# Optimization experiments

Measured on AMD Instinct MI355X. Metric: run time of the kernel, lower is better.

## Reference

```python
import jax, jax.numpy as jnp
import numpy as np

HEADS, DIM_HEAD, DIM = 12, 64, 768
H = W = 32
N = H * W
B = 4


def _ln(x, g, b, eps=1e-5):
    mu = x.mean(-1, keepdims=True)
    var = ((x - mu) ** 2).mean(-1, keepdims=True)
    return (x - mu) / jnp.sqrt(var + eps) * g + b


def _get_epipolar(k, src_c2w, target_c2w, h=H, w=W):
    # Faithful port of Epipolar_Attention.get_epipolar, without the (hw*hw,3) repeat
    # materialization (uses broadcasting for the pairwise cross product instead).
    b = k.shape[0]
    Wf = h * 16.0 / 9.0
    k = k.astype(jnp.float32)
    k = k.at[:, 0, :].multiply(Wf).at[:, 1, :].multiply(float(h))
    k = k.at[:, 0, 2].set(h / 2.0).at[:, 1, 2].set(h / 2.0)
    ii, jj = jnp.meshgrid(jnp.arange(h), jnp.arange(w), indexing='ij')
    # after the torch column swap: (col, row, 1)
    coords = jnp.stack([jj.ravel(), ii.ravel(), jnp.ones(h * w, jnp.int32)], axis=1).astype(jnp.float32)  # [hw,3]
    k3 = k[:, :3, :3]
    src_r, src_t = src_c2w[:, :3, :3].astype(jnp.float32), src_c2w[:, :3, 3].astype(jnp.float32)
    tgt_r, tgt_t = target_c2w[:, :3, :3].astype(jnp.float32), target_c2w[:, :3, 3].astype(jnp.float32)
    tgt_rinv = jnp.linalg.inv(tgt_r)
    fx, fy = k3[:, 0, 0][:, None], k3[:, 1, 1][:, None]
    cx, cy = k3[:, 0, 2][:, None], k3[:, 1, 2][:, None]
    nc = jnp.stack([(coords[None, :, 0] - cx) / fx,
                    (coords[None, :, 1] - cy) / fy,
                    jnp.broadcast_to(coords[None, :, 2], (b, h * w))], axis=-1)  # [b,hw,3]
    p3w = jnp.einsum('bij,bnj->bni', src_r, nc) + src_t[:, None]
    p2 = jnp.einsum('bij,bnj->bni', tgt_rinv, p3w) - tgt_t[:, None]  # target_w2c_t = -target_c2w_t
    pij_un = jnp.einsum('bij,bnj->bni', k3, p2)                      # [b,hw,3]
    pij = pij_un / (pij_un[..., -1:] + 1e-6)
    o2 = jnp.einsum('bij,bj->bi', tgt_rinv, src_t) - tgt_t           # origin projected
    oij = jnp.einsum('bij,bj->bi', k3, o2)
    oij = oij / oij[..., -1:]
    oi_to_pi = pij - oij[:, None]                # [b,hw,3]
    oi_to_coord = coords[None] - oij[:, None]    # [b,hw,3]
    cr = jnp.cross(oi_to_pi[:, :, None, :], oi_to_coord[:, None, :, :])  # [b,hw,hw,3]
    area = jnp.sqrt((cr * cr).sum(-1))
    vlen = jnp.sqrt((oi_to_pi * oi_to_pi).sum(-1))[:, :, None]
    dist = area / vlen
    dw = 1.0 - jax.nn.sigmoid(50.0 * (dist - 0.5))
    row_max = dw.max(-1, keepdims=True)
    return jnp.where(row_max < 0.5, 1.0, dw)     # rows with max<0.5 are set to all-ones


def setup_inputs():
    key = jax.random.key(0)
    ks = jax.random.split(key, 16)
    s = 0.02
    x = jax.random.normal(ks[0], (B, N, DIM), jnp.float32)
    src_encode = jax.random.normal(ks[1], (B, N, DIM), jnp.float32)
    intrinsic = (jnp.zeros((B, 4, 4), jnp.float32)
                 .at[:, 0, 0].set(1.0).at[:, 1, 1].set(1.0)
                 .at[:, 0, 2].set(0.5).at[:, 1, 2].set(0.5)
                 .at[:, 2, 2].set(1.0).at[:, 3, 3].set(1.0))
    R = jnp.eye(3, dtype=jnp.float32) + 0.1 * jax.random.normal(ks[2], (2, B, 3, 3), jnp.float32)
    t = 0.5 * jax.random.normal(ks[3], (2, B, 3), jnp.float32)
    c2w = (jnp.zeros((2, B, 4, 4), jnp.float32)
           .at[:, :, :3, :3].set(R).at[:, :, :3, 3].set(t).at[:, :, 3, 3].set(1.0))
    hd = HEADS * DIM_HEAD
    w_ = lambda k_, shp: s * jax.random.normal(k_, shp, jnp.float32)
    return dict(
        x=x, src_encode=src_encode, intrinsic=intrinsic, c2w=c2w,
        lnq_g=jnp.ones(DIM), lnq_b=jnp.zeros(DIM), Wq=w_(ks[4], (DIM, hd)), bq=jnp.zeros(hd),
        lnk_g=jnp.ones(DIM), lnk_b=jnp.zeros(DIM), Wk=w_(ks[5], (DIM, hd)), bk=jnp.zeros(hd),
        lnv_g=jnp.ones(DIM), lnv_b=jnp.zeros(DIM), Wv=w_(ks[6], (DIM, hd)), bv=jnp.zeros(hd),
        Wp=w_(ks[7], (hd, DIM)), bp=jnp.zeros(DIM),
        pre_g=jnp.ones(DIM), pre_b=jnp.zeros(DIM),
        W1=w_(ks[8], (DIM, 2 * DIM)), b1=jnp.zeros(2 * DIM),
        W2=w_(ks[9], (2 * DIM, DIM)), b2=jnp.zeros(DIM),
        post_g=jnp.ones(DIM), post_b=jnp.zeros(DIM))


def reference(x, src_encode, intrinsic, c2w, lnq_g, lnq_b, Wq, bq, lnk_g, lnk_b, Wk, bk,
              lnv_g, lnv_b, Wv, bv, Wp, bp, pre_g, pre_b, W1, b1, W2, b2, post_g, post_b):
    b, n, _ = x.shape
    scale = DIM_HEAD ** -0.5
    split = lambda t_: t_.reshape(b, n, HEADS, DIM_HEAD).transpose(0, 2, 1, 3)  # [b,m,n,d]
    q = split(_ln(x, lnq_g, lnq_b) @ Wq + bq)
    k = split(_ln(src_encode, lnk_g, lnk_b) @ Wk + bk)
    v = split(_ln(src_encode, lnv_g, lnv_b) @ Wv + bv)
    scores = scale * jnp.einsum('bmqd,bmkd->bmqk', q, k)
    e1 = _get_epipolar(intrinsic, c2w[1], c2w[0])                    # do_epipolar
    e2 = jnp.swapaxes(_get_epipolar(intrinsic, c2w[0], c2w[1]), 1, 2)  # bidirectional (transposed)
    wmap = e1 * e2                                                   # [b,n,n], shared across heads
    att = jax.nn.softmax(scores * wmap[:, None], axis=-1)
    a = jnp.einsum('bmqk,bmkd->bmqd', att, v).transpose(0, 2, 1, 3).reshape(b, n, HEADS * DIM_HEAD)
    z = _ln(a @ Wp + bp, pre_g, pre_b)
    z = z + (jax.nn.gelu(z @ W1 + b1, approximate=False) @ W2 + b2)  # torch nn.GELU = exact erf
    z = _ln(z, post_g, post_b)
    wm_full = jnp.broadcast_to(wmap[:, None], (b, HEADS, n, n)).reshape(b * HEADS, n, n)
    return z, wm_full
```

## Files before the change

kernel.cpp:

```cpp
#include <hip/hip_runtime.h>
#include <hip/hip_bf16.h>

typedef unsigned short u16;
typedef __attribute__((ext_vector_type(4))) unsigned short u16x4;
typedef __attribute__((ext_vector_type(8))) unsigned short u16x8;
typedef __attribute__((ext_vector_type(8))) short s16x8;
typedef __attribute__((ext_vector_type(4))) float f32x4;

#define HEADS 12
#define NSEQ 1024
#define DIMM 768
#define DHEAD 64

__device__ __forceinline__ float b2f(u16 h) {
  union { unsigned u; float f; } v; v.u = ((unsigned)h) << 16; return v.f;
}
__device__ __forceinline__ u16 f2b(float f) {
  union { float f; unsigned u; } v; v.f = f;
  unsigned r = v.u + 0x7fffu + ((v.u >> 16) & 1u);
  return (u16)(r >> 16);
}
__device__ __forceinline__ void gl_lds16(const u16* g, u16* l) {
  __builtin_amdgcn_global_load_lds(
      (const __attribute__((address_space(1))) void*)g,
      (__attribute__((address_space(3))) void*)l, 16, 0, 0);
}

template<bool GELU, bool RESID>
__device__ __forceinline__ void gemm_body(
    const u16* __restrict__ A, const u16* __restrict__ BT,
    const float* __restrict__ bias, const u16* __restrict__ resid,
    const float* __restrict__ rg, const float* __restrict__ rb,
    u16* __restrict__ C, int K, int lda, int ldb, int ldc,
    int m0, int n0, u16* As, u16* Bs)
{
  const int tid = threadIdx.x;
  const int lane = tid & 63;
  const int wv = tid >> 6;
  const int wm0 = (wv >> 1) * 64;
  const int wn0 = (wv & 1) * 64;
  const int l15 = lane & 15;
  const int quad = lane >> 4;
  const int srow = lane >> 2;
  const int scol = (lane & 3) * 8;

  f32x4 acc[4][4];
  #pragma unroll
  for (int i = 0; i < 4; ++i)
    #pragma unroll
    for (int j = 0; j < 4; ++j)
      acc[i][j] = {0.f, 0.f, 0.f, 0.f};

  const u16* Ab = A + (long)(m0 + wv * 32 + srow) * lda + scol;
  const u16* Bb = BT + (long)(n0 + wv * 32 + srow) * ldb + scol;
  u16* AsW = As + (wv * 32) * 32;
  u16* BsW = Bs + (wv * 32) * 32;

  #pragma unroll
  for (int t = 0; t < 2; ++t) {
    gl_lds16(Ab + (long)t * 16 * lda, AsW + t * 16 * 32);
    gl_lds16(Bb + (long)t * 16 * ldb, BsW + t * 16 * 32);
  }

  int cur = 0;
  for (int k0 = 0; k0 < K; k0 += 32) {
    __syncthreads();
    if (k0 + 32 < K) {
      const int nxt = cur ^ 1;
      #pragma unroll
      for (int t = 0; t < 2; ++t) {
        gl_lds16(Ab + (k0 + 32) + (long)t * 16 * lda, AsW + nxt * 4096 + t * 16 * 32);
        gl_lds16(Bb + (k0 + 32) + (long)t * 16 * ldb, BsW + nxt * 4096 + t * 16 * 32);
      }
    }
    const u16* Ac = As + cur * 4096;
    const u16* Bc = Bs + cur * 4096;
    s16x8 af[4], bfr[4];
    #pragma unroll
    for (int i = 0; i < 4; ++i)
      af[i] = *(const s16x8*)&Ac[(wm0 + i * 16 + l15) * 32 + quad * 8];
    #pragma unroll
    for (int j = 0; j < 4; ++j)
      bfr[j] = *(const s16x8*)&Bc[(wn0 + j * 16 + l15) * 32 + quad * 8];
    #pragma unroll
    for (int i = 0; i < 4; ++i)
      #pragma unroll
      for (int j = 0; j < 4; ++j)
        acc[i][j] = __builtin_amdgcn_mfma_f32_16x16x32_bf16(af[i], bfr[j], acc[i][j], 0, 0, 0);
    cur ^= 1;
  }

  #pragma unroll
  for (int i = 0; i < 4; ++i)
    #pragma unroll
    for (int j = 0; j < 4; ++j) {
      const int col = n0 + wn0 + j * 16 + l15;
      const float bvv = bias[col];
      #pragma unroll
      for (int v = 0; v < 4; ++v) {
        const int row = m0 + wm0 + i * 16 + quad * 4 + v;
        float val = acc[i][j][v] + bvv;
        if (GELU) val = 0.5f * val * (1.0f + erff(val * 0.70710678118654752440f));
        if (RESID) val += b2f(resid[(long)row * ldc + col]) * rg[col] + rb[col];
        C[(long)row * ldc + col] = f2b(val);
      }
    }
}

template<bool GELU, bool RESID>
__global__ __launch_bounds__(256)
void gemm_one(const u16* __restrict__ A, const u16* __restrict__ BT,
              const float* __restrict__ bias, const u16* __restrict__ resid,
              const float* __restrict__ rg, const float* __restrict__ rb,
              u16* __restrict__ C, int K, int lda, int ldb, int ldc)
{
  __shared__ u16 As[8192], Bs[8192];
  gemm_body<GELU, RESID>(A, BT, bias, resid, rg, rb, C, K, lda, ldb, ldc,
                         blockIdx.x * 128, blockIdx.y * 128, As, Bs);
}

__global__ __launch_bounds__(256)
void gemm_qkv(const u16* __restrict__ nx, const u16* __restrict__ ns,
              const u16* __restrict__ qT, const u16* __restrict__ kvT,
              const float* __restrict__ bqf, const float* __restrict__ bkvf,
              u16* __restrict__ qb, u16* __restrict__ kvb)
{
  __shared__ u16 As[8192], Bs[8192];
  const int z = blockIdx.z;
  if (z == 0)
    gemm_body<false, false>(nx, qT, bqf, nullptr, nullptr, nullptr, qb,
                            768, 768, 768, 768,
                            blockIdx.x * 128, blockIdx.y * 128, As, Bs);
  else
    gemm_body<false, false>(ns, kvT, bkvf, nullptr, nullptr, nullptr, kvb,
                            768, 768, 768, 1536,
                            blockIdx.x * 128, (z - 1) * 768 + blockIdx.y * 128, As, Bs);
}

__global__ __launch_bounds__(256, 3)
void fattn(const u16* __restrict__ qb, const u16* __restrict__ kvb,
           const u16* __restrict__ vT, const u16* __restrict__ wm,
           u16* __restrict__ outA)
{
  __shared__ u16 Qs[2 * 64 * 32];
  __shared__ u16 Ks[2 * 64 * 32];
  __shared__ u16 Vs[2 * 64 * 32];
  __shared__ u16 Ws[64][72];
  __shared__ u16 Ps[64][72];

  const int bh = blockIdx.y;
  const int b = bh / HEADS, h = bh - b * HEADS;
  const int q0 = blockIdx.x * 64;
  const int tid = threadIdx.x;
  const int lane = tid & 63;
  const int wv = tid >> 6;
  const int l15 = lane & 15;
  const int quad = lane >> 4;
  const int srow = lane >> 2;
  const int scol = (lane & 3) * 8;

  const u16* Qg = qb + ((long)b * NSEQ + q0) * DIMM + h * DHEAD;
  const u16* Kg = kvb + (long)b * NSEQ * 1536 + h * DHEAD;
  const u16* Vg = vT + (long)bh * DHEAD * NSEQ;
  const u16* Wg = wm + ((long)b * NSEQ + q0) * NSEQ;

  #pragma unroll
  for (int h2 = 0; h2 < 2; ++h2)
    gl_lds16(Qg + (long)(wv * 16 + srow) * DIMM + h2 * 32 + scol,
             Qs + (h2 * 64 + wv * 16) * 32);

  f32x4 Sacc[4], Oacc[4];
  float mrow[4], lrow[4];
  #pragma unroll
  for (int j = 0; j < 4; ++j) {
    Oacc[j] = {0.f, 0.f, 0.f, 0.f};
    mrow[j] = -3.0e38f;
    lrow[j] = 0.f;
  }
  s16x8 qf[2];

  for (int kt = 0; kt < 16; ++kt) {
    __syncthreads();
    #pragma unroll
    for (int h2 = 0; h2 < 2; ++h2) {
      gl_lds16(Kg + (long)(kt * 64 + wv * 16 + srow) * 1536 + h2 * 32 + scol,
               Ks + (h2 * 64 + wv * 16) * 32);
      gl_lds16(Vg + (long)(wv * 16 + srow) * NSEQ + kt * 64 + h2 * 32 + scol,
               Vs + (h2 * 64 + wv * 16) * 32);
    }
    #pragma unroll
    for (int t = 0; t < 2; ++t) {
      const int col = (lane & 3) * 16 + t * 8;
      u16x8 wvv = *(const u16x8*)&Wg[(long)(wv * 16 + srow) * NSEQ + kt * 64 + col];
      *(u16x8*)&Ws[wv * 16 + srow][col] = wvv;
    }
    __syncthreads();

    if (kt == 0) {
      qf[0] = *(const s16x8*)&Qs[(0 * 64 + wv * 16 + l15) * 32 + quad * 8];
      qf[1] = *(const s16x8*)&Qs[(1 * 64 + wv * 16 + l15) * 32 + quad * 8];
    }

    #pragma unroll
    for (int j = 0; j < 4; ++j) Sacc[j] = {0.f, 0.f, 0.f, 0.f};
    #pragma unroll
    for (int j = 0; j < 4; ++j)
      #pragma unroll
      for (int h2 = 0; h2 < 2; ++h2) {
        s16x8 kf = *(const s16x8*)&Ks[(h2 * 64 + j * 16 + l15) * 32 + quad * 8];
        Sacc[j] = __builtin_amdgcn_mfma_f32_16x16x32_bf16(qf[h2], kf, Sacc[j], 0, 0, 0);
      }

    #pragma unroll
    for (int j = 0; j < 4; ++j)
      #pragma unroll
      for (int v = 0; v < 4; ++v)
        Sacc[j][v] *= b2f(Ws[wv * 16 + quad * 4 + v][j * 16 + l15]);
    #pragma unroll
    for (int v = 0; v < 4; ++v) {
      float tm = fmaxf(fmaxf(Sacc[0][v], Sacc[1][v]), fmaxf(Sacc[2][v], Sacc[3][v]));
      tm = fmaxf(tm, __shfl_xor(tm, 1));
      tm = fmaxf(tm, __shfl_xor(tm, 2));
      tm = fmaxf(tm, __shfl_xor(tm, 4));
      tm = fmaxf(tm, __shfl_xor(tm, 8));
      const float mnew = fmaxf(mrow[v], tm);
      const float al = __expf(mrow[v] - mnew);
      float rs = 0.f;
      #pragma unroll
      for (int j = 0; j < 4; ++j) {
        const float e = __expf(Sacc[j][v] - mnew);
        Sacc[j][v] = e;
        rs += e;
      }
      rs += __shfl_xor(rs, 1);
      rs += __shfl_xor(rs, 2);
      rs += __shfl_xor(rs, 4);
      rs += __shfl_xor(rs, 8);
      lrow[v] = lrow[v] * al + rs;
      mrow[v] = mnew;
      #pragma unroll
      for (int jn = 0; jn < 4; ++jn) Oacc[jn][v] *= al;
    }
    #pragma unroll
    for (int j = 0; j < 4; ++j)
      #pragma unroll
      for (int v = 0; v < 4; ++v)
        Ps[wv * 16 + quad * 4 + v][j * 16 + l15] = f2b(Sacc[j][v]);

    #pragma unroll
    for (int h2 = 0; h2 < 2; ++h2) {
      s16x8 af = *(const s16x8*)&Ps[wv * 16 + l15][h2 * 32 + quad * 8];
      #pragma unroll
      for (int jn = 0; jn < 4; ++jn) {
        s16x8 vf = *(const s16x8*)&Vs[(h2 * 64 + jn * 16 + l15) * 32 + quad * 8];
        Oacc[jn] = __builtin_amdgcn_mfma_f32_16x16x32_bf16(af, vf, Oacc[jn], 0, 0, 0);
      }
    }
  }

  #pragma unroll
  for (int v = 0; v < 4; ++v) {
    const int row = q0 + wv * 16 + quad * 4 + v;
    const float inv = 1.0f / lrow[v];
    #pragma unroll
    for (int jn = 0; jn < 4; ++jn)
      outA[((long)(b * NSEQ + row)) * DIMM + h * DHEAD + jn * 16 + l15] =
          f2b(Oacc[jn][v] * inv);
  }
}

template<bool F32IN>
__global__ __launch_bounds__(256)
void norm_k(const void* __restrict__ in, u16* __restrict__ out)
{
  const long base = (long)blockIdx.x * DIMM;
  const int tid = threadIdx.x;
  __shared__ float s1[8], s2[8];
  float v0, v1, v2;
  if (F32IN) {
    const float* p = (const float*)in + base;
    v0 = p[tid]; v1 = p[tid + 256]; v2 = p[tid + 512];
  } else {
    const u16* p = (const u16*)in + base;
    v0 = b2f(p[tid]); v1 = b2f(p[tid + 256]); v2 = b2f(p[tid + 512]);
  }
  float s = v0 + v1 + v2;
  #pragma unroll
  for (int off = 32; off; off >>= 1) s += __shfl_down(s, off);
  const int lane = tid & 63, wid = tid >> 6;
  if (!lane) s1[wid] = s;
  __syncthreads();
  if (!tid) s1[4] = s1[0] + s1[1] + s1[2] + s1[3];
  __syncthreads();
  const float mu = s1[4] / 768.0f;
  float d0 = v0 - mu, d1 = v1 - mu, d2 = v2 - mu;
  float sq = d0 * d0 + d1 * d1 + d2 * d2;
  #pragma unroll
  for (int off = 32; off; off >>= 1) sq += __shfl_down(sq, off);
  if (!lane) s2[wid] = sq;
  __syncthreads();
  if (!tid) s2[4] = s2[0] + s2[1] + s2[2] + s2[3];
  __syncthreads();
  const float rstd = 1.0f / sqrtf(s2[4] / 768.0f + 1e-5f);
  u16* o = out + base;
  o[tid]       = f2b(d0 * rstd);
  o[tid + 256] = f2b(d1 * rstd);
  o[tid + 512] = f2b(d2 * rstd);
}

__global__ __launch_bounds__(256)
void ln_final(const u16* __restrict__ in, const float* __restrict__ g,
              const float* __restrict__ bb, float* __restrict__ out)
{
  const long base = (long)blockIdx.x * DIMM;
  const int tid = threadIdx.x;
  __shared__ float s1[8], s2[8];
  const u16* p = in + base;
  float v0 = b2f(p[tid]), v1 = b2f(p[tid + 256]), v2 = b2f(p[tid + 512]);
  float s = v0 + v1 + v2;
  #pragma unroll
  for (int off = 32; off; off >>= 1) s += __shfl_down(s, off);
  const int lane = tid & 63, wid = tid >> 6;
  if (!lane) s1[wid] = s;
  __syncthreads();
  if (!tid) s1[4] = s1[0] + s1[1] + s1[2] + s1[3];
  __syncthreads();
  const float mu = s1[4] / 768.0f;
  float d0 = v0 - mu, d1 = v1 - mu, d2 = v2 - mu;
  float sq = d0 * d0 + d1 * d1 + d2 * d2;
  #pragma unroll
  for (int off = 32; off; off >>= 1) sq += __shfl_down(sq, off);
  if (!lane) s2[wid] = sq;
  __syncthreads();
  if (!tid) s2[4] = s2[0] + s2[1] + s2[2] + s2[3];
  __syncthreads();
  const float rstd = 1.0f / sqrtf(s2[4] / 768.0f + 1e-5f);
  float* o = out + base;
  o[tid]       = d0 * rstd * g[tid]       + bb[tid];
  o[tid + 256] = d1 * rstd * g[tid + 256] + bb[tid + 256];
  o[tid + 512] = d2 * rstd * g[tid + 512] + bb[tid + 512];
}

__global__ __launch_bounds__(256)
void trans_all(const float* w0, const float* w1, const float* w2,
               const float* w3, const float* w4, const float* w5,
               const float* gq, const float* gk, const float* gv, const float* gp,
               u16* d0, u16* d12, u16* d3, u16* d4, u16* d5)
{
  const float* src; const float* g; u16* dst; int R, C; float sc = 1.0f;
  switch (blockIdx.z) {
    case 0: src = w0; g = gq; dst = d0;  R = 768;  C = 768;  sc = 0.125f; break;
    case 1: src = w1; g = gk; dst = d12; R = 768;  C = 768;  break;
    case 2: src = w2; g = gv; dst = d12 + 768 * 768; R = 768; C = 768; break;
    case 3: src = w3; g = nullptr; dst = d3; R = 768;  C = 768;  break;
    case 4: src = w4; g = gp; dst = d4; R = 768;  C = 1536; break;
    default: src = w5; g = nullptr; dst = d5; R = 1536; C = 768; break;
  }
  const int c0 = blockIdx.x * 32;
  const int r0 = blockIdx.y * 32;
  if (c0 >= C || r0 >= R) return;
  __shared__ u16 t[32][36];
  const int tid = threadIdx.x;
  const int i = tid >> 3;
  const int j4 = (tid & 7) * 4;
  const float rs = (g ? g[r0 + i] : 1.0f) * sc;
  #pragma unroll
  for (int jj = 0; jj < 4; ++jj)
    t[i][j4 + jj] = f2b(src[(long)(r0 + i) * C + c0 + j4 + jj] * rs);
  __syncthreads();
  u16x4 ov;
  #pragma unroll
  for (int jj = 0; jj < 4; ++jj) ov[jj] = t[j4 + jj][i];
  *(u16x4*)&dst[(long)(c0 + i) * R + r0 + j4] = ov;
}

__global__ __launch_bounds__(256)
void biasfold(const float* Wq, const float* Wk, const float* Wv, const float* W1,
              const float* bq, const float* bk, const float* bv, const float* b1,
              const float* lnqb, const float* lnkb, const float* lnvb, const float* preb,
              float* obq, float* obkv, float* ob1)
{
  const int y = blockIdx.y;
  const int c = blockIdx.x * 256 + threadIdx.x;
  const float* W; const float* bln; const float* bw; float* out;
  int C; float sc = 1.0f;
  switch (y) {
    case 0: W = Wq; bln = lnqb; bw = bq; out = obq;        C = 768;  sc = 0.125f; break;
    case 1: W = Wk; bln = lnkb; bw = bk; out = obkv;       C = 768;  break;
    case 2: W = Wv; bln = lnvb; bw = bv; out = obkv + 768; C = 768;  break;
    default: W = W1; bln = preb; bw = b1; out = ob1;       C = 1536; break;
  }
  if (c >= C) return;
  float s = bw[c];
  for (int r = 0; r < 768; ++r) s += bln[r] * W[(long)r * C + c];
  out[c] = s * sc;
}

__global__ __launch_bounds__(256)
void v_transpose(const u16* __restrict__ kvb, u16* __restrict__ vT)
{
  __shared__ u16 t[64][72];
  const int z = blockIdx.y;
  const int b = z / HEADS, h = z - b * HEADS;
  const int n0 = blockIdx.x * 64;
  const int tid = threadIdx.x;
  const int i = tid >> 2;
  const int jb = (tid & 3) * 16;
  const u16* src = kvb + (long)(b * NSEQ + n0 + i) * 1536 + 768 + h * DHEAD + jb;
  *(u16x8*)&t[i][jb]     = *(const u16x8*)&src[0];
  *(u16x8*)&t[i][jb + 8] = *(const u16x8*)&src[8];
  __syncthreads();
  const int dd = tid >> 2;
  const int nb = (tid & 3) * 16;
  u16x8 o0, o1;
  #pragma unroll
  for (int nn = 0; nn < 8; ++nn) { o0[nn] = t[nb + nn][dd]; o1[nn] = t[nb + 8 + nn][dd]; }
  u16* dst = vT + ((long)z * DHEAD + dd) * NSEQ + n0 + nb;
  *(u16x8*)&dst[0] = o0;
  *(u16x8*)&dst[8] = o1;
}

__global__ void epi_setup(const float* __restrict__ intr, const float* __restrict__ c2w,
                          float* __restrict__ u4, float* __restrict__ oijb)
{
  const int db = blockIdx.x;
  const int d = db >> 2, b = db & 3;
  __shared__ float S[36];
  if (threadIdx.x == 0) {
    const int sidx = (d == 0) ? 1 : 0;
    const int tidx = 1 - sidx;
    float k3[9], sr[9], st[3], tr[9], tt[3];
    const float Wf = 32.0f * 16.0f / 9.0f;
    for (int j = 0; j < 3; ++j) {
      k3[j]     = intr[(b * 4 + 0) * 4 + j] * Wf;
      k3[3 + j] = intr[(b * 4 + 1) * 4 + j] * 32.0f;
      k3[6 + j] = intr[(b * 4 + 2) * 4 + j];
    }
    k3[2] = 16.0f; k3[5] = 16.0f;
    for (int i = 0; i < 3; ++i) {
      for (int j = 0; j < 3; ++j) {
        sr[i * 3 + j] = c2w[((sidx * 4 + b) * 4 + i) * 4 + j];
        tr[i * 3 + j] = c2w[((tidx * 4 + b) * 4 + i) * 4 + j];
      }
      st[i] = c2w[((sidx * 4 + b) * 4 + i) * 4 + 3];
      tt[i] = c2w[((tidx * 4 + b) * 4 + i) * 4 + 3];
    }
    double a = tr[0], bb_ = tr[1], c = tr[2];
    double dd2 = tr[3], e = tr[4], f = tr[5];
    double g2 = tr[6], h2 = tr[7], i2 = tr[8];
    double det = a * (e * i2 - f * h2) - bb_ * (dd2 * i2 - f * g2) + c * (dd2 * h2 - e * g2);
    double inv[9] = {
      (e * i2 - f * h2), (c * h2 - bb_ * i2), (bb_ * f - c * e),
      (f * g2 - dd2 * i2), (a * i2 - c * g2), (c * dd2 - a * f),
      (dd2 * h2 - e * g2), (bb_ * g2 - a * h2), (a * e - bb_ * dd2)
    };
    float tri[9];
    for (int t2 = 0; t2 < 9; ++t2) tri[t2] = (float)(inv[t2] / det);
    float o2[3], oij[3];
    for (int i3 = 0; i3 < 3; ++i3)
      o2[i3] = tri[i3 * 3] * st[0] + tri[i3 * 3 + 1] * st[1] + tri[i3 * 3 + 2] * st[2] - tt[i3];
    for (int i3 = 0; i3 < 3; ++i3)
      oij[i3] = k3[i3 * 3] * o2[0] + k3[i3 * 3 + 1] * o2[1] + k3[i3 * 3 + 2] * o2[2];
    const float ozf = oij[2];
    oij[0] = oij[0] / ozf; oij[1] = oij[1] / ozf; oij[2] = ozf / ozf;
    for (int t2 = 0; t2 < 9; ++t2) { S[t2] = k3[t2]; S[9 + t2] = sr[t2]; S[21 + t2] = tri[t2]; }
    for (int t2 = 0; t2 < 3; ++t2) { S[18 + t2] = st[t2]; S[30 + t2] = tt[t2]; S[33 + t2] = oij[t2]; }
    oijb[db * 4 + 0] = oij[0]; oijb[db * 4 + 1] = oij[1]; oijb[db * 4 + 2] = oij[2];
    oijb[db * 4 + 3] = 0.f;
  }
  __syncthreads();
  for (int n = threadIdx.x; n < 1024; n += blockDim.x) {
    const float ncx = ((float)(n & 31) - S[2]) / S[0];
    const float ncy = ((float)(n >> 5) - S[5]) / S[4];
    const float p0 = S[9]  * ncx + S[10] * ncy + S[11] + S[18];
    const float p1 = S[12] * ncx + S[13] * ncy + S[14] + S[19];
    const float p2 = S[15] * ncx + S[16] * ncy + S[17] + S[20];
    const float q0 = S[21] * p0 + S[22] * p1 + S[23] * p2 - S[30];
    const float q1 = S[24] * p0 + S[25] * p1 + S[26] * p2 - S[31];
    const float q2 = S[27] * p0 + S[28] * p1 + S[29] * p2 - S[32];
    const float w0 = S[0] * q0 + S[1] * q1 + S[2] * q2;
    const float w1 = S[3] * q0 + S[4] * q1 + S[5] * q2;
    const float w2 = S[6] * q0 + S[7] * q1 + S[8] * q2;
    const float pz = w2 + 1e-6f;
    const float ux = w0 / pz - S[33];
    const float uy = w1 / pz - S[34];
    const float uz = w2 / pz - S[35];
    const float vlen = sqrtf(ux * ux + uy * uy + uz * uz);
    f32x4 uo = {ux, uy, uz, vlen};
    *(f32x4*)&u4[((long)db * 1024 + n) * 4] = uo;
  }
}

__global__ __launch_bounds__(256)
void epi_dw(const float* __restrict__ u4, const float* __restrict__ oijb,
            float* __restrict__ dw)
{
  const int rowid = blockIdx.x;
  const int db = rowid >> 10;
  const f32x4 U = *(const f32x4*)&u4[(long)rowid * 4];
  const float ox = oijb[db * 4 + 0];
  const float oy = oijb[db * 4 + 1];
  const float oz = oijb[db * 4 + 2];
  const int tid = threadIdx.x;
  __shared__ float red[8];
  float vals[4];
  float mx = -1e30f;
  #pragma unroll
  for (int i = 0; i < 4; ++i) {
    const int m = tid + i * 256;
    const float cx = (float)(m & 31) - ox;
    const float cy = (float)(m >> 5) - oy;
    const float cz = 1.0f - oz;
    const float crx = U.y * cz - U.z * cy;
    const float cry = U.z * cx - U.x * cz;
    const float crz = U.x * cy - U.y * cx;
    const float area = sqrtf(crx * crx + cry * cry + crz * crz);
    const float dist = area / U.w;
    const float t = 50.0f * (dist - 0.5f);
    const float dwv = 1.0f - 1.0f / (1.0f + __expf(-t));
    vals[i] = dwv;
    mx = fmaxf(mx, dwv);
  }
  #pragma unroll
  for (int off = 32; off; off >>= 1) mx = fmaxf(mx, __shfl_down(mx, off));
  const int lane = tid & 63, wid = tid >> 6;
  if (!lane) red[wid] = mx;
  __syncthreads();
  if (!tid) red[4] = fmaxf(fmaxf(red[0], red[1]), fmaxf(red[2], red[3]));
  __syncthreads();
  const bool fill1 = red[4] < 0.5f;
  float* out = dw + (long)rowid * 1024;
  #pragma unroll
  for (int i = 0; i < 4; ++i)
    out[tid + i * 256] = fill1 ? 1.0f : vals[i];
}

__global__ __launch_bounds__(256)
void epi_wmap(const float* __restrict__ dw, u16* __restrict__ wm,
              float* __restrict__ wm_full)
{
  __shared__ float tb[32][33];
  const int b = blockIdx.z;
  const int q0 = blockIdx.x * 32;
  const int k0 = blockIdx.y * 32;
  const int tid = threadIdx.x;
  const int i = tid >> 3;
  const int j4 = (tid & 7) * 4;
  const float* d1 = dw + ((long)(4 + b) * 1024 + (k0 + i)) * 1024 + q0 + j4;
  #pragma unroll
  for (int jj = 0; jj < 4; ++jj) tb[i][j4 + jj] = d1[jj];
  __syncthreads();
  const float* d0 = dw + ((long)b * 1024 + (q0 + i)) * 1024 + k0 + j4;
  u16x4 pk;
  f32x4 wf;
  #pragma unroll
  for (int jj = 0; jj < 4; ++jj) {
    const float w = d0[jj] * tb[j4 + jj][i];
    wf[jj] = w;
    pk[jj] = f2b(w);
  }
  *(u16x4*)&wm[((long)b * 1024 + q0 + i) * 1024 + k0 + j4] = pk;
  #pragma unroll
  for (int h = 0; h < HEADS; ++h)
    *(f32x4*)&wm_full[((long)(b * HEADS + h) * 1024 + q0 + i) * 1024 + k0 + j4] = wf;
}

extern "C" void kernel_launch(void* const* d_in, const int* in_sizes, int n_in,
                              void* d_out, int out_size, void* d_ws, size_t ws_size,
                              hipStream_t stream)
{
  (void)in_sizes; (void)n_in; (void)out_size; (void)ws_size;
  const float* x     = (const float*)d_in[0];
  const float* src   = (const float*)d_in[1];
  const float* intr  = (const float*)d_in[2];
  const float* c2w   = (const float*)d_in[3];
  const float* lnq_g = (const float*)d_in[4];
  const float* lnq_b = (const float*)d_in[5];
  const float* Wq    = (const float*)d_in[6];
  const float* bq    = (const float*)d_in[7];
  const float* lnk_g = (const float*)d_in[8];
  const float* lnk_b = (const float*)d_in[9];
  const float* Wk    = (const float*)d_in[10];
  const float* bk    = (const float*)d_in[11];
  const float* lnv_g = (const float*)d_in[12];
  const float* lnv_b = (const float*)d_in[13];
  const float* Wv    = (const float*)d_in[14];
  const float* bv    = (const float*)d_in[15];
  const float* Wp    = (const float*)d_in[16];
  const float* bp    = (const float*)d_in[17];
  const float* pre_g = (const float*)d_in[18];
  const float* pre_b = (const float*)d_in[19];
  const float* W1    = (const float*)d_in[20];
  const float* b1    = (const float*)d_in[21];
  const float* W2    = (const float*)d_in[22];
  const float* b2    = (const float*)d_in[23];
  const float* post_g= (const float*)d_in[24];
  const float* post_b= (const float*)d_in[25];

  char* ws = (char*)d_ws;
  size_t off = 0;
  auto alloc = [&](size_t bytes) -> char* {
    char* p = ws + off;
    off = (off + bytes + 255) & ~(size_t)255;
    return p;
  };
  const size_t SEQD = (size_t)4096 * 768 * 2;

  u16* WqT  = (u16*)alloc(768 * 768 * 2);
  u16* WkvT = (u16*)alloc((size_t)1536 * 768 * 2);
  u16* WpT  = (u16*)alloc(768 * 768 * 2);
  u16* W1T  = (u16*)alloc(768 * 1536 * 2);
  u16* W2T  = (u16*)alloc(1536 * 768 * 2);
  float* bqf  = (float*)alloc(768 * 4);
  float* bkvf = (float*)alloc(1536 * 4);
  float* b1f  = (float*)alloc(1536 * 4);
  char* pool = alloc(6 * SEQD);
  float* u4   = (float*)alloc(8 * 1024 * 4 * 4);
  float* oijb = (float*)alloc(8 * 4 * 4);
  u16* wmapb  = (u16*)alloc((size_t)4 * 1024 * 1024 * 2);
  float* dwbuf = (float*)alloc((size_t)8 * 1024 * 1024 * 4);

  u16* S0 = (u16*)pool;
  u16* S1 = (u16*)(pool + SEQD);
  u16* S2 = (u16*)(pool + 2 * SEQD);
  u16* S3 = (u16*)(pool + 3 * SEQD);
  u16* S5 = (u16*)(pool + 5 * SEQD);

  float* out_z  = (float*)d_out;
  float* out_wm = (float*)d_out + (size_t)4 * 1024 * 768;

  trans_all<<<dim3(48, 48, 6), 256, 0, stream>>>(
      Wq, Wk, Wv, Wp, W1, W2, lnq_g, lnk_g, lnv_g, pre_g,
      WqT, WkvT, WpT, W1T, W2T);
  biasfold<<<dim3(6, 4), 256, 0, stream>>>(
      Wq, Wk, Wv, W1, bq, bk, bv, b1, lnq_b, lnk_b, lnv_b, pre_b,
      bqf, bkvf, b1f);

  epi_setup<<<8, 128, 0, stream>>>(intr, c2w, u4, oijb);
  epi_dw<<<8192, 256, 0, stream>>>(u4, oijb, dwbuf);
  epi_wmap<<<dim3(32, 32, 4), 256, 0, stream>>>(dwbuf, wmapb, out_wm);

  norm_k<true><<<4096, 256, 0, stream>>>(x, S0);
  norm_k<true><<<4096, 256, 0, stream>>>(src, S1);

  gemm_qkv<<<dim3(32, 6, 3), 256, 0, stream>>>(S0, S1, WqT, WkvT, bqf, bkvf, S2, S3);

  v_transpose<<<dim3(16, 48), 256, 0, stream>>>(S3, S5);

  fattn<<<dim3(16, 48), 256, 0, stream>>>(S2, S3, S5, wmapb, S0);

  gemm_one<false, false><<<dim3(32, 6), 256, 0, stream>>>(
      S0, WpT, bp, nullptr, nullptr, nullptr, S1, 768, 768, 768, 768);

  norm_k<false><<<4096, 256, 0, stream>>>(S1, S2);

  gemm_one<true, false><<<dim3(32, 12), 256, 0, stream>>>(
      S2, W1T, b1f, nullptr, nullptr, nullptr, S3, 768, 768, 768, 1536);

  gemm_one<false, true><<<dim3(32, 6), 256, 0, stream>>>(
      S3, W2T, b2, S2, pre_g, pre_b, S5, 1536, 1536, 1536, 768);

  ln_final<<<4096, 256, 0, stream>>>(S5, post_g, post_b, out_z);
}
```

Measured before the change: 555.8 us.

## Fuse small kernels: V transpose into QKV GEMM epilogue, merge norms, setup and bias passes

The V projection epilogue now writes V directly in the transposed per-head layout, so the separate v_transpose kernel goes away, and K is stored in its own 768-wide buffer. The two input LayerNorms become one launch, the bias fold moves into the weight transpose kernel as an extra z-slice, and the epipolar setup is recomputed per row inside epi_dw. The aim is fewer launches and less intermediate traffic. In exchange, epi_dw repeats the setup math in every block, and the transposed V stores are 8-byte scattered writes.

```diff
diff --git a/kernel.cpp b/kernel.cpp
--- a/kernel.cpp
+++ b/kernel.cpp
@@ -26,13 +26,10 @@
       (__attribute__((address_space(3))) void*)l, 16, 0, 0);
 }
 
-template<bool GELU, bool RESID>
-__device__ __forceinline__ void gemm_body(
+__device__ __forceinline__ void gemm_acc(
     const u16* __restrict__ A, const u16* __restrict__ BT,
-    const float* __restrict__ bias, const u16* __restrict__ resid,
-    const float* __restrict__ rg, const float* __restrict__ rb,
-    u16* __restrict__ C, int K, int lda, int ldb, int ldc,
-    int m0, int n0, u16* As, u16* Bs)
+    int K, int lda, int ldb, int m0, int n0,
+    u16* As, u16* Bs, f32x4 acc[4][4])
 {
   const int tid = threadIdx.x;
   const int lane = tid & 63;
@@ -44,13 +41,6 @@
   const int srow = lane >> 2;
   const int scol = (lane & 3) * 8;
 
-  f32x4 acc[4][4];
-  #pragma unroll
-  for (int i = 0; i < 4; ++i)
-    #pragma unroll
-    for (int j = 0; j < 4; ++j)
-      acc[i][j] = {0.f, 0.f, 0.f, 0.f};
-
   const u16* Ab = A + (long)(m0 + wv * 32 + srow) * lda + scol;
   const u16* Bb = BT + (long)(n0 + wv * 32 + srow) * ldb + scol;
   u16* AsW = As + (wv * 32) * 32;
@@ -89,7 +79,29 @@
         acc[i][j] = __builtin_amdgcn_mfma_f32_16x16x32_bf16(af[i], bfr[j], acc[i][j], 0, 0, 0);
     cur ^= 1;
   }
-
+}
+
+template<bool GELU, bool RESID>
+__global__ __launch_bounds__(256)
+void gemm_one(const u16* __restrict__ A, const u16* __restrict__ BT,
+              const float* __restrict__ bias, const u16* __restrict__ resid,
+              const float* __restrict__ rg, const float* __restrict__ rb,
+              u16* __restrict__ C, int K, int lda, int ldb, int ldc)
+{
+  __shared__ u16 As[8192], Bs[8192];
+  f32x4 acc[4][4];
+  #pragma unroll
+  for (int i = 0; i < 4; ++i)
+    #pragma unroll
+    for (int j = 0; j < 4; ++j)
+      acc[i][j] = {0.f, 0.f, 0.f, 0.f};
+  const int m0 = blockIdx.x * 128, n0 = blockIdx.y * 128;
+  gemm_acc(A, BT, K, lda, ldb, m0, n0, As, Bs, acc);
+
+  const int lane = threadIdx.x & 63;
+  const int wv = threadIdx.x >> 6;
+  const int wm0 = (wv >> 1) * 64, wn0 = (wv & 1) * 64;
+  const int l15 = lane & 15, quad = lane >> 4;
   #pragma unroll
   for (int i = 0; i < 4; ++i)
     #pragma unroll
@@ -107,38 +119,65 @@
     }
 }
 
-template<bool GELU, bool RESID>
-__global__ __launch_bounds__(256)
-void gemm_one(const u16* __restrict__ A, const u16* __restrict__ BT,
-              const float* __restrict__ bias, const u16* __restrict__ resid,
-              const float* __restrict__ rg, const float* __restrict__ rb,
-              u16* __restrict__ C, int K, int lda, int ldb, int ldc)
-{
-  __shared__ u16 As[8192], Bs[8192];
-  gemm_body<GELU, RESID>(A, BT, bias, resid, rg, rb, C, K, lda, ldb, ldc,
-                         blockIdx.x * 128, blockIdx.y * 128, As, Bs);
-}
-
 __global__ __launch_bounds__(256)
 void gemm_qkv(const u16* __restrict__ nx, const u16* __restrict__ ns,
               const u16* __restrict__ qT, const u16* __restrict__ kvT,
               const float* __restrict__ bqf, const float* __restrict__ bkvf,
-              u16* __restrict__ qb, u16* __restrict__ kvb)
+              u16* __restrict__ qb, u16* __restrict__ kb, u16* __restrict__ vT)
 {
   __shared__ u16 As[8192], Bs[8192];
   const int z = blockIdx.z;
-  if (z == 0)
-    gemm_body<false, false>(nx, qT, bqf, nullptr, nullptr, nullptr, qb,
-                            768, 768, 768, 768,
-                            blockIdx.x * 128, blockIdx.y * 128, As, Bs);
-  else
-    gemm_body<false, false>(ns, kvT, bkvf, nullptr, nullptr, nullptr, kvb,
-                            768, 768, 768, 1536,
-                            blockIdx.x * 128, (z - 1) * 768 + blockIdx.y * 128, As, Bs);
+  const int m0 = blockIdx.x * 128;
+  const int n0 = blockIdx.y * 128 + ((z == 2) ? 768 : 0);
+  const u16* Aptr = (z == 0) ? nx : ns;
+  const u16* Bptr = (z == 0) ? qT : kvT;
+  f32x4 acc[4][4];
+  #pragma unroll
+  for (int i = 0; i < 4; ++i)
+    #pragma unroll
+    for (int j = 0; j < 4; ++j)
+      acc[i][j] = {0.f, 0.f, 0.f, 0.f};
+  gemm_acc(Aptr, Bptr, 768, 768, 768, m0, n0, As, Bs, acc);
+
+  const int lane = threadIdx.x & 63;
+  const int wv = threadIdx.x >> 6;
+  const int wm0 = (wv >> 1) * 64, wn0 = (wv & 1) * 64;
+  const int l15 = lane & 15, quad = lane >> 4;
+
+  if (z < 2) {
+    u16* C = (z == 0) ? qb : kb;
+    const float* bias = (z == 0) ? bqf : bkvf;
+    #pragma unroll
+    for (int i = 0; i < 4; ++i)
+      #pragma unroll
+      for (int j = 0; j < 4; ++j) {
+        const int col = n0 + wn0 + j * 16 + l15;
+        const float bvv = bias[col];
+        #pragma unroll
+        for (int v = 0; v < 4; ++v) {
+          const int row = m0 + wm0 + i * 16 + quad * 4 + v;
+          C[(long)row * 768 + col] = f2b(acc[i][j][v] + bvv);
+        }
+      }
+  } else {
+    const int b = m0 >> 10;
+    #pragma unroll
+    for (int i = 0; i < 4; ++i)
+      #pragma unroll
+      for (int j = 0; j < 4; ++j) {
+        const int col = (n0 - 768) + wn0 + j * 16 + l15;
+        const float bvv = bkvf[768 + col];
+        const int row0 = (m0 + wm0 + i * 16 + quad * 4) & 1023;
+        u16x4 pk;
+        #pragma unroll
+        for (int v = 0; v < 4; ++v) pk[v] = f2b(acc[i][j][v] + bvv);
+        *(u16x4*)&vT[((long)(b * HEADS + (col >> 6)) * 64 + (col & 63)) * 1024 + row0] = pk;
+      }
+  }
 }
 
 __global__ __launch_bounds__(256, 3)
-void fattn(const u16* __restrict__ qb, const u16* __restrict__ kvb,
+void fattn(const u16* __restrict__ qb, const u16* __restrict__ kb,
            const u16* __restrict__ vT, const u16* __restrict__ wm,
            u16* __restrict__ outA)
 {
@@ -160,7 +199,7 @@
   const int scol = (lane & 3) * 8;
 
   const u16* Qg = qb + ((long)b * NSEQ + q0) * DIMM + h * DHEAD;
-  const u16* Kg = kvb + (long)b * NSEQ * 1536 + h * DHEAD;
+  const u16* Kg = kb + (long)b * NSEQ * DIMM + h * DHEAD;
   const u16* Vg = vT + (long)bh * DHEAD * NSEQ;
   const u16* Wg = wm + ((long)b * NSEQ + q0) * NSEQ;
 
@@ -183,7 +222,7 @@
     __syncthreads();
     #pragma unroll
     for (int h2 = 0; h2 < 2; ++h2) {
-      gl_lds16(Kg + (long)(kt * 64 + wv * 16 + srow) * 1536 + h2 * 32 + scol,
+      gl_lds16(Kg + (long)(kt * 64 + wv * 16 + srow) * DIMM + h2 * 32 + scol,
                Ks + (h2 * 64 + wv * 16) * 32);
       gl_lds16(Vg + (long)(wv * 16 + srow) * NSEQ + kt * 64 + h2 * 32 + scol,
                Vs + (h2 * 64 + wv * 16) * 32);
@@ -269,21 +308,48 @@
   }
 }
 
-template<bool F32IN>
-__global__ __launch_bounds__(256)
-void norm_k(const void* __restrict__ in, u16* __restrict__ out)
+__global__ __launch_bounds__(256)
+void norm_xs(const float* __restrict__ x, const float* __restrict__ src,
+             u16* __restrict__ ox, u16* __restrict__ osrc)
+{
+  const int which = blockIdx.x >> 12;
+  const long row = blockIdx.x & 4095;
+  const float* in = (which ? src : x) + row * DIMM;
+  u16* out = (which ? osrc : ox) + row * DIMM;
+  const int tid = threadIdx.x;
+  __shared__ float s1[8], s2[8];
+  float v0 = in[tid], v1 = in[tid + 256], v2 = in[tid + 512];
+  float s = v0 + v1 + v2;
+  #pragma unroll
+  for (int off = 32; off; off >>= 1) s += __shfl_down(s, off);
+  const int lane = tid & 63, wid = tid >> 6;
+  if (!lane) s1[wid] = s;
+  __syncthreads();
+  if (!tid) s1[4] = s1[0] + s1[1] + s1[2] + s1[3];
+  __syncthreads();
+  const float mu = s1[4] / 768.0f;
+  float d0 = v0 - mu, d1 = v1 - mu, d2 = v2 - mu;
+  float sq = d0 * d0 + d1 * d1 + d2 * d2;
+  #pragma unroll
+  for (int off = 32; off; off >>= 1) sq += __shfl_down(sq, off);
+  if (!lane) s2[wid] = sq;
+  __syncthreads();
+  if (!tid) s2[4] = s2[0] + s2[1] + s2[2] + s2[3];
+  __syncthreads();
+  const float rstd = 1.0f / sqrtf(s2[4] / 768.0f + 1e-5f);
+  out[tid]       = f2b(d0 * rstd);
+  out[tid + 256] = f2b(d1 * rstd);
+  out[tid + 512] = f2b(d2 * rstd);
+}
+
+__global__ __launch_bounds__(256)
+void norm_b(const u16* __restrict__ in, u16* __restrict__ out)
 {
   const long base = (long)blockIdx.x * DIMM;
   const int tid = threadIdx.x;
   __shared__ float s1[8], s2[8];
-  float v0, v1, v2;
-  if (F32IN) {
-    const float* p = (const float*)in + base;
-    v0 = p[tid]; v1 = p[tid + 256]; v2 = p[tid + 512];
-  } else {
-    const u16* p = (const u16*)in + base;
-    v0 = b2f(p[tid]); v1 = b2f(p[tid + 256]); v2 = b2f(p[tid + 512]);
-  }
+  const u16* p = in + base;
+  float v0 = b2f(p[tid]), v1 = b2f(p[tid + 256]), v2 = b2f(p[tid + 512]);
   float s = v0 + v1 + v2;
   #pragma unroll
   for (int off = 32; off; off >>= 1) s += __shfl_down(s, off);
@@ -342,13 +408,35 @@
 }
 
 __global__ __launch_bounds__(256)
-void trans_all(const float* w0, const float* w1, const float* w2,
-               const float* w3, const float* w4, const float* w5,
-               const float* gq, const float* gk, const float* gv, const float* gp,
-               u16* d0, u16* d12, u16* d3, u16* d4, u16* d5)
-{
+void trans_bias(const float* w0, const float* w1, const float* w2,
+                const float* w3, const float* w4, const float* w5,
+                const float* gq, const float* gk, const float* gv, const float* gp,
+                const float* bq, const float* bk, const float* bv, const float* b1,
+                const float* lnqb, const float* lnkb, const float* lnvb, const float* preb,
+                u16* d0, u16* d12, u16* d3, u16* d4, u16* d5,
+                float* obq, float* obkv, float* ob1)
+{
+  const int zz = blockIdx.z;
+  if (zz == 6) {
+    const int y = blockIdx.y;
+    if (y >= 4) return;
+    const int c = blockIdx.x * 256 + threadIdx.x;
+    const float* W; const float* bln; const float* bw; float* out;
+    int C; float sc = 1.0f;
+    switch (y) {
+      case 0: W = w0; bln = lnqb; bw = bq; out = obq;        C = 768;  sc = 0.125f; break;
+      case 1: W = w1; bln = lnkb; bw = bk; out = obkv;       C = 768;  break;
+      case 2: W = w2; bln = lnvb; bw = bv; out = obkv + 768; C = 768;  break;
+      default: W = w4; bln = preb; bw = b1; out = ob1;       C = 1536; break;
+    }
+    if (c >= C) return;
+    float s = bw[c];
+    for (int r = 0; r < 768; ++r) s += bln[r] * W[(long)r * C + c];
+    out[c] = s * sc;
+    return;
+  }
   const float* src; const float* g; u16* dst; int R, C; float sc = 1.0f;
-  switch (blockIdx.z) {
+  switch (zz) {
     case 0: src = w0; g = gq; dst = d0;  R = 768;  C = 768;  sc = 0.125f; break;
     case 1: src = w1; g = gk; dst = d12; R = 768;  C = 768;  break;
     case 2: src = w2; g = gv; dst = d12 + 768 * 768; R = 768; C = 768; break;
@@ -375,55 +463,12 @@
 }
 
 __global__ __launch_bounds__(256)
-void biasfold(const float* Wq, const float* Wk, const float* Wv, const float* W1,
-              const float* bq, const float* bk, const float* bv, const float* b1,
-              const float* lnqb, const float* lnkb, const float* lnvb, const float* preb,
-              float* obq, float* obkv, float* ob1)
-{
-  const int y = blockIdx.y;
-  const int c = blockIdx.x * 256 + threadIdx.x;
-  const float* W; const float* bln; const float* bw; float* out;
-  int C; float sc = 1.0f;
-  switch (y) {
-    case 0: W = Wq; bln = lnqb; bw = bq; out = obq;        C = 768;  sc = 0.125f; break;
-    case 1: W = Wk; bln = lnkb; bw = bk; out = obkv;       C = 768;  break;
-    case 2: W = Wv; bln = lnvb; bw = bv; out = obkv + 768; C = 768;  break;
-    default: W = W1; bln = preb; bw = b1; out = ob1;       C = 1536; break;
-  }
-  if (c >= C) return;
-  float s = bw[c];
-  for (int r = 0; r < 768; ++r) s += bln[r] * W[(long)r * C + c];
-  out[c] = s * sc;
-}
-
-__global__ __launch_bounds__(256)
-void v_transpose(const u16* __restrict__ kvb, u16* __restrict__ vT)
-{
-  __shared__ u16 t[64][72];
-  const int z = blockIdx.y;
-  const int b = z / HEADS, h = z - b * HEADS;
-  const int n0 = blockIdx.x * 64;
-  const int tid = threadIdx.x;
-  const int i = tid >> 2;
-  const int jb = (tid & 3) * 16;
-  const u16* src = kvb + (long)(b * NSEQ + n0 + i) * 1536 + 768 + h * DHEAD + jb;
-  *(u16x8*)&t[i][jb]     = *(const u16x8*)&src[0];
-  *(u16x8*)&t[i][jb + 8] = *(const u16x8*)&src[8];
-  __syncthreads();
-  const int dd = tid >> 2;
-  const int nb = (tid & 3) * 16;
-  u16x8 o0, o1;
-  #pragma unroll
-  for (int nn = 0; nn < 8; ++nn) { o0[nn] = t[nb + nn][dd]; o1[nn] = t[nb + 8 + nn][dd]; }
-  u16* dst = vT + ((long)z * DHEAD + dd) * NSEQ + n0 + nb;
-  *(u16x8*)&dst[0] = o0;
-  *(u16x8*)&dst[8] = o1;
-}
-
-__global__ void epi_setup(const float* __restrict__ intr, const float* __restrict__ c2w,
-                          float* __restrict__ u4, float* __restrict__ oijb)
-{
-  const int db = blockIdx.x;
+void epi_dw(const float* __restrict__ intr, const float* __restrict__ c2w,
+            float* __restrict__ dw)
+{
+  const int rowid = blockIdx.x;
+  const int db = rowid >> 10;
+  const int n = rowid & 1023;
   const int d = db >> 2, b = db & 3;
   __shared__ float S[36];
   if (threadIdx.x == 0) {
@@ -465,42 +510,27 @@
     oij[0] = oij[0] / ozf; oij[1] = oij[1] / ozf; oij[2] = ozf / ozf;
     for (int t2 = 0; t2 < 9; ++t2) { S[t2] = k3[t2]; S[9 + t2] = sr[t2]; S[21 + t2] = tri[t2]; }
     for (int t2 = 0; t2 < 3; ++t2) { S[18 + t2] = st[t2]; S[30 + t2] = tt[t2]; S[33 + t2] = oij[t2]; }
-    oijb[db * 4 + 0] = oij[0]; oijb[db * 4 + 1] = oij[1]; oijb[db * 4 + 2] = oij[2];
-    oijb[db * 4 + 3] = 0.f;
-  }
-  __syncthreads();
-  for (int n = threadIdx.x; n < 1024; n += blockDim.x) {
-    const float ncx = ((float)(n & 31) - S[2]) / S[0];
-    const float ncy = ((float)(n >> 5) - S[5]) / S[4];
-    const float p0 = S[9]  * ncx + S[10] * ncy + S[11] + S[18];
-    const float p1 = S[12] * ncx + S[13] * ncy + S[14] + S[19];
-    const float p2 = S[15] * ncx + S[16] * ncy + S[17] + S[20];
-    const float q0 = S[21] * p0 + S[22] * p1 + S[23] * p2 - S[30];
-    const float q1 = S[24] * p0 + S[25] * p1 + S[26] * p2 - S[31];
-    const float q2 = S[27] * p0 + S[28] * p1 + S[29] * p2 - S[32];
-    const float w0 = S[0] * q0 + S[1] * q1 + S[2] * q2;
-    const float w1 = S[3] * q0 + S[4] * q1 + S[5] * q2;
-    const float w2 = S[6] * q0 + S[7] * q1 + S[8] * q2;
-    const float pz = w2 + 1e-6f;
-    const float ux = w0 / pz - S[33];
-    const float uy = w1 / pz - S[34];
-    const float uz = w2 / pz - S[35];
-    const float vlen = sqrtf(ux * ux + uy * uy + uz * uz);
-    f32x4 uo = {ux, uy, uz, vlen};
-    *(f32x4*)&u4[((long)db * 1024 + n) * 4] = uo;
-  }
-}
-
-__global__ __launch_bounds__(256)
-void epi_dw(const float* __restrict__ u4, const float* __restrict__ oijb,
-            float* __restrict__ dw)
-{
-  const int rowid = blockIdx.x;
-  const int db = rowid >> 10;
-  const f32x4 U = *(const f32x4*)&u4[(long)rowid * 4];
-  const float ox = oijb[db * 4 + 0];
-  const float oy = oijb[db * 4 + 1];
-  const float oz = oijb[db * 4 + 2];
+  }
+  __syncthreads();
+
+  const float ncx = ((float)(n & 31) - S[2]) / S[0];
+  const float ncy = ((float)(n >> 5) - S[5]) / S[4];
+  const float p0 = S[9]  * ncx + S[10] * ncy + S[11] + S[18];
+  const float p1 = S[12] * ncx + S[13] * ncy + S[14] + S[19];
+  const float p2 = S[15] * ncx + S[16] * ncy + S[17] + S[20];
+  const float q0 = S[21] * p0 + S[22] * p1 + S[23] * p2 - S[30];
+  const float q1 = S[24] * p0 + S[25] * p1 + S[26] * p2 - S[31];
+  const float q2 = S[27] * p0 + S[28] * p1 + S[29] * p2 - S[32];
+  const float w0 = S[0] * q0 + S[1] * q1 + S[2] * q2;
+  const float w1 = S[3] * q0 + S[4] * q1 + S[5] * q2;
+  const float w2 = S[6] * q0 + S[7] * q1 + S[8] * q2;
+  const float pz = w2 + 1e-6f;
+  const float Ux = w0 / pz - S[33];
+  const float Uy = w1 / pz - S[34];
+  const float Uz = w2 / pz - S[35];
+  const float vlen = sqrtf(Ux * Ux + Uy * Uy + Uz * Uz);
+  const float ox = S[33], oy = S[34], oz = S[35];
+
   const int tid = threadIdx.x;
   __shared__ float red[8];
   float vals[4];
@@ -511,11 +541,11 @@
     const float cx = (float)(m & 31) - ox;
     const float cy = (float)(m >> 5) - oy;
     const float cz = 1.0f - oz;
-    const float crx = U.y * cz - U.z * cy;
-    const float cry = U.z * cx - U.x * cz;
-    const float crz = U.x * cy - U.y * cx;
+    const float crx = Uy * cz - Uz * cy;
+    const float cry = Uz * cx - Ux * cz;
+    const float crz = Ux * cy - Uy * cx;
     const float area = sqrtf(crx * crx + cry * cry + crz * crz);
-    const float dist = area / U.w;
+    const float dist = area / vlen;
     const float t = 50.0f * (dist - 0.5f);
     const float dwv = 1.0f - 1.0f / (1.0f + __expf(-t));
     vals[i] = dwv;
@@ -615,8 +645,6 @@
   float* bkvf = (float*)alloc(1536 * 4);
   float* b1f  = (float*)alloc(1536 * 4);
   char* pool = alloc(6 * SEQD);
-  float* u4   = (float*)alloc(8 * 1024 * 4 * 4);
-  float* oijb = (float*)alloc(8 * 4 * 4);
   u16* wmapb  = (u16*)alloc((size_t)4 * 1024 * 1024 * 2);
   float* dwbuf = (float*)alloc((size_t)8 * 1024 * 1024 * 4);
 
@@ -624,35 +652,31 @@
   u16* S1 = (u16*)(pool + SEQD);
   u16* S2 = (u16*)(pool + 2 * SEQD);
   u16* S3 = (u16*)(pool + 3 * SEQD);
+  u16* S4 = (u16*)(pool + 4 * SEQD);
   u16* S5 = (u16*)(pool + 5 * SEQD);
 
   float* out_z  = (float*)d_out;
   float* out_wm = (float*)d_out + (size_t)4 * 1024 * 768;
 
-  trans_all<<<dim3(48, 48, 6), 256, 0, stream>>>(
+  trans_bias<<<dim3(48, 48, 7), 256, 0, stream>>>(
       Wq, Wk, Wv, Wp, W1, W2, lnq_g, lnk_g, lnv_g, pre_g,
-      WqT, WkvT, WpT, W1T, W2T);
-  biasfold<<<dim3(6, 4), 256, 0, stream>>>(
-      Wq, Wk, Wv, W1, bq, bk, bv, b1, lnq_b, lnk_b, lnv_b, pre_b,
-      bqf, bkvf, b1f);
-
-  epi_setup<<<8, 128, 0, stream>>>(intr, c2w, u4, oijb);
-  epi_dw<<<8192, 256, 0, stream>>>(u4, oijb, dwbuf);
+      bq, bk, bv, b1, lnq_b, lnk_b, lnv_b, pre_b,
+      WqT, WkvT, WpT, W1T, W2T, bqf, bkvf, b1f);
+
+  epi_dw<<<8192, 256, 0, stream>>>(intr, c2w, dwbuf);
   epi_wmap<<<dim3(32, 32, 4), 256, 0, stream>>>(dwbuf, wmapb, out_wm);
 
-  norm_k<true><<<4096, 256, 0, stream>>>(x, S0);
-  norm_k<true><<<4096, 256, 0, stream>>>(src, S1);
-
-  gemm_qkv<<<dim3(32, 6, 3), 256, 0, stream>>>(S0, S1, WqT, WkvT, bqf, bkvf, S2, S3);
-
-  v_transpose<<<dim3(16, 48), 256, 0, stream>>>(S3, S5);
-
-  fattn<<<dim3(16, 48), 256, 0, stream>>>(S2, S3, S5, wmapb, S0);
+  norm_xs<<<8192, 256, 0, stream>>>(x, src, S0, S1);
+
+  gemm_qkv<<<dim3(32, 6, 3), 256, 0, stream>>>(
+      S0, S1, WqT, WkvT, bqf, bkvf, S2, S3, S4);
+
+  fattn<<<dim3(16, 48), 256, 0, stream>>>(S2, S3, S4, wmapb, S0);
 
   gemm_one<false, false><<<dim3(32, 6), 256, 0, stream>>>(
       S0, WpT, bp, nullptr, nullptr, nullptr, S1, 768, 768, 768, 768);
 
-  norm_k<false><<<4096, 256, 0, stream>>>(S1, S2);
+  norm_b<<<4096, 256, 0, stream>>>(S1, S2);
 
   gemm_one<true, false><<<dim3(32, 12), 256, 0, stream>>>(
       S2, W1T, b1f, nullptr, nullptr, nullptr, S3, 768, 768, 768, 1536);
```

Result: no change. 564.4 us (+1.5%).
